# Performance work log

Measured on AMD Instinct MI355X. Metric: run time of the kernel, lower is better.

## Reference

```python
import jax, jax.numpy as jnp
import numpy as np

B, S, H = 1, 2048, 2048
NH = 16            # num attention heads
QLR = 1536         # q_lora_rank
KVLR = 512         # kv_lora_rank
DR = 64            # qk_rope_head_dim
DN = 128           # qk_nope_head_dim
DV = 128           # v_head_dim
DQK = DN + DR      # qk_head_dim = 192
EPS = 1e-6


def rmsnorm(x, w):
    xf = x.astype(jnp.float32)
    var = jnp.mean(xf * xf, axis=-1, keepdims=True)
    return (xf * jax.lax.rsqrt(var + EPS)).astype(x.dtype) * w


def rotate_half(x):
    d = x.shape[-1] // 2
    return jnp.concatenate([-x[..., d:], x[..., :d]], axis=-1)


def rope_interleave(x, cos, sin):
    # x: [b, h, s, d]; de-interleave pairs (even dims -> first half, odd -> second)
    b, h, s, d = x.shape
    x = x.reshape(b, h, s, d // 2, 2).swapaxes(-1, -2).reshape(b, h, s, d)
    return x * cos + rotate_half(x) * sin


def setup_inputs() -> dict:
    key = jax.random.key(0)
    ks = jax.random.split(key, 8)
    std = 0.02
    hidden_states = jax.random.normal(ks[0], (B, S, H), jnp.float32)
    # real rotary cos/sin for a 64-dim rope slice
    pos = jnp.arange(S, dtype=jnp.float32)
    inv_freq = 1.0 / (10000.0 ** (jnp.arange(0, DR, 2, dtype=jnp.float32) / DR))
    ang = pos[:, None] * inv_freq[None, :]            # [S, DR//2]
    emb = jnp.concatenate([ang, ang], axis=-1)        # [S, DR]
    cos = jnp.broadcast_to(jnp.cos(emb)[None], (B, S, DR)).astype(jnp.float32)
    sin = jnp.broadcast_to(jnp.sin(emb)[None], (B, S, DR)).astype(jnp.float32)
    # weights stored [in, out]
    wq_a = jax.random.normal(ks[1], (H, QLR), jnp.float32) * std
    q_ln = jnp.ones((QLR,), jnp.float32)
    wq_b = jax.random.normal(ks[2], (QLR, NH * DQK), jnp.float32) * std
    wkv_a = jax.random.normal(ks[3], (H, KVLR + DR), jnp.float32) * std
    kv_ln = jnp.ones((KVLR,), jnp.float32)
    wkv_b = jax.random.normal(ks[4], (KVLR, NH * (DN + DV)), jnp.float32) * std
    wo = jax.random.normal(ks[5], (NH * DV, H), jnp.float32) * std
    return {"hidden_states": hidden_states, "cos": cos, "sin": sin,
            "wq_a": wq_a, "q_ln": q_ln, "wq_b": wq_b,
            "wkv_a": wkv_a, "kv_ln": kv_ln, "wkv_b": wkv_b, "wo": wo}


def reference(hidden_states, cos, sin, wq_a, q_ln, wq_b, wkv_a, kv_ln, wkv_b, wo):
    b, s, _ = hidden_states.shape
    # low-rank Q: a-proj -> RMSNorm -> b-proj
    q = rmsnorm(hidden_states @ wq_a, q_ln) @ wq_b           # [b, s, NH*DQK]
    q = q.reshape(b, s, NH, DQK).transpose(0, 2, 1, 3)       # [b, NH, s, DQK]
    q_pass, q_rot = q[..., :DN], q[..., DN:]
    # compressed KV with shared rope key
    ckv = hidden_states @ wkv_a                               # [b, s, KVLR+DR]
    kv_c, k_rot = ckv[..., :KVLR], ckv[..., KVLR:]
    kv = (rmsnorm(kv_c, kv_ln) @ wkv_b).reshape(b, s, NH, DN + DV).transpose(0, 2, 1, 3)
    k_pass, v = kv[..., :DN], kv[..., DN:]
    k_rot = k_rot[:, None, :, :]                              # [b, 1, s, DR]
    cos4, sin4 = cos[:, None], sin[:, None]
    q_rot = rope_interleave(q_rot, cos4, sin4)
    k_rot = rope_interleave(k_rot, cos4, sin4)
    k_rot = jnp.broadcast_to(k_rot, (b, NH, s, DR))
    qs = jnp.concatenate([q_pass, q_rot], axis=-1)            # [b, NH, s, DQK]
    ks_ = jnp.concatenate([k_pass, k_rot], axis=-1)
    scaling = DQK ** -0.5
    scores = jnp.einsum('bhqd,bhkd->bhqk', qs, ks_) * scaling
    causal = jnp.tril(jnp.ones((s, s), bool))
    scores = jnp.where(causal, scores, jnp.finfo(scores.dtype).min)
    probs = jax.nn.softmax(scores.astype(jnp.float32), axis=-1).astype(qs.dtype)
    out = jnp.einsum('bhqk,bhkd->bhqd', probs, v)             # [b, NH, s, DV]
    out = out.transpose(0, 2, 1, 3).reshape(b, s, NH * DV)
    return out @ wo
```

## Files before the change

### kernel.cpp

```cpp
#include <hip/hip_runtime.h>
#include <hip/hip_bf16.h>
#include <stdint.h>

#define S_    2048
#define H_    2048
#define NH_   16
#define QLR_  1536
#define KVLR_ 512
#define DR_   64
#define DN_   128
#define DV_   128
#define DQK_  192
#define QW_   (NH_*DQK_)
#define KVW_  (NH_*(DN_+DV_))
#define CKVW_ (KVLR_+DR_)

typedef __attribute__((ext_vector_type(8))) short short8;
typedef __attribute__((ext_vector_type(4))) float floatx4;

__device__ __forceinline__ unsigned short f2bf(float f) {
    unsigned u = __float_as_uint(f);
    unsigned r = u + 0x7fffu + ((u >> 16) & 1u);
    return (unsigned short)(r >> 16);
}
__device__ __forceinline__ float bf2f(unsigned short h) {
    return __uint_as_float(((unsigned)h) << 16);
}
__device__ __forceinline__ void store_out(float* p, float v) { *p = v; }
__device__ __forceinline__ void store_out(unsigned short* p, float v) { *p = f2bf(v); }

typedef const __attribute__((address_space(1))) unsigned int* gas_ptr;
typedef __attribute__((address_space(3))) unsigned int* las_ptr;
__device__ __forceinline__ void gload16(const void* g, void* l) {
    __builtin_amdgcn_global_load_lds((gas_ptr)g, (las_ptr)l, 16, 0, 0);
}

__device__ __forceinline__ int xcd_swz(int orig, int nwg) {
    int q8 = nwg >> 3, r8 = nwg & 7;
    int xcd = orig & 7, jj = orig >> 3;
    return (xcd < r8 ? xcd * (q8 + 1) : r8 * (q8 + 1) + (xcd - r8) * q8) + jj;
}

#define GEMM_STAGE(b, k0) do {                                               \
        _Pragma("unroll")                                                    \
        for (int sub = 0; sub < 2; ++sub) {                                  \
            int m = tid >> 2, k8 = tid & 3;                                  \
            gload16(A + (size_t)(bm + m) * lda + (k0) + sub * 32 + k8 * 8,   \
                    &As[b][sub][tid * 8]);                                   \
        }                                                                    \
        _Pragma("unroll")                                                    \
        for (int sub = 0; sub < 2; ++sub)                                    \
            _Pragma("unroll")                                                \
            for (int j = 0; j < BN / 64; ++j) {                              \
                int ch = j * 256 + tid;                                      \
                int n = ch >> 2, k8 = ch & 3;                                \
                int nrow = bn + n; if (nrow >= N) nrow = N - 1;              \
                gload16(Bt + (size_t)nrow * K + (k0) + sub * 32 + k8 * 8,    \
                        &Bs[b][sub][ch * 8]);                                \
            }                                                                \
    } while (0)

#define GEMM_COMPUTE_SUB(sub) do {                                           \
        short8 a[2], b[NFR];                                                 \
        _Pragma("unroll")                                                    \
        for (int mi = 0; mi < 2; ++mi)                                       \
            a[mi] = *(const short8*)&As[cur][sub][(wm + mi * 16 + cc) * 32 + g * 8]; \
        _Pragma("unroll")                                                    \
        for (int ni = 0; ni < NFR; ++ni)                                     \
            b[ni] = *(const short8*)&Bs[cur][sub][(wn + ni * 16 + cc) * 32 + g * 8]; \
        __builtin_amdgcn_s_setprio(1);                                       \
        _Pragma("unroll")                                                    \
        for (int mi = 0; mi < 2; ++mi)                                       \
            _Pragma("unroll")                                                \
            for (int ni = 0; ni < NFR; ++ni)                                 \
                acc[mi][ni] = __builtin_amdgcn_mfma_f32_16x16x32_bf16(       \
                    a[mi], b[ni], acc[mi][ni], 0, 0, 0);                     \
        __builtin_amdgcn_s_setprio(0);                                       \
    } while (0)

template <typename OutT, int BN>
__global__ __launch_bounds__(256) void gemm_bf16_db(
    const unsigned short* __restrict__ A, const unsigned short* __restrict__ Bt,
    OutT* __restrict__ C, int M, int N, int K, int lda, int ldc)
{
    constexpr int NFR = BN / 32;
    __shared__ unsigned short As[2][2][64 * 32];
    __shared__ unsigned short Bs[2][2][BN * 32];

    const int tid = threadIdx.x;
    const int l = tid & 63;
    const int g = l >> 4, cc = l & 15;
    const int w = tid >> 6;
    const int wm = (w >> 1) * 32, wn = (w & 1) * (BN / 2);

    const int nwg = gridDim.x * gridDim.y;
    const int wg = xcd_swz(blockIdx.y * gridDim.x + blockIdx.x, nwg);
    const int bm = (wg / gridDim.x) * 64;
    const int bn = (wg % gridDim.x) * BN;

    floatx4 acc[2][NFR];
#pragma unroll
    for (int i = 0; i < 2; i++)
#pragma unroll
        for (int j = 0; j < NFR; j++) acc[i][j] = (floatx4){0.f, 0.f, 0.f, 0.f};

    GEMM_STAGE(0, 0);
    __syncthreads();
    int cur = 0;

    for (int k0 = 0; k0 < K; k0 += 64) {
        if (k0 + 64 < K) GEMM_STAGE(cur ^ 1, k0 + 64);
        GEMM_COMPUTE_SUB(0);
        GEMM_COMPUTE_SUB(1);
        __syncthreads();
        cur ^= 1;
    }

#pragma unroll
    for (int mi = 0; mi < 2; ++mi)
#pragma unroll
        for (int ni = 0; ni < NFR; ++ni)
#pragma unroll
            for (int i = 0; i < 4; ++i) {
                int row = bm + wm + mi * 16 + g * 4 + i;
                int col = bn + wn + ni * 16 + cc;
                if (col < N) store_out(&C[(size_t)row * ldc + col], acc[mi][ni][i]);
            }
}

__global__ __launch_bounds__(256) void gemm_bf16_dual(
    const unsigned short* __restrict__ A, const unsigned short* __restrict__ Bt,
    float* __restrict__ C0, float* __restrict__ C1,
    int M, int N, int K, int lda, int ldc0, int ldc1)
{
    constexpr int BN = 128;
    constexpr int NFR = 4;
    __shared__ unsigned short As[2][2][64 * 32];
    __shared__ unsigned short Bs[2][2][BN * 32];

    const int tid = threadIdx.x;
    const int l = tid & 63;
    const int g = l >> 4, cc = l & 15;
    const int w = tid >> 6;
    const int wm = (w >> 1) * 32, wn = (w & 1) * (BN / 2);

    const int nwg = gridDim.x * gridDim.y;
    const int wg = xcd_swz(blockIdx.y * gridDim.x + blockIdx.x, nwg);
    const int bm = (wg / gridDim.x) * 64;
    const int bn = (wg % gridDim.x) * BN;

    floatx4 acc[2][NFR];
#pragma unroll
    for (int i = 0; i < 2; i++)
#pragma unroll
        for (int j = 0; j < NFR; j++) acc[i][j] = (floatx4){0.f, 0.f, 0.f, 0.f};

    GEMM_STAGE(0, 0);
    __syncthreads();
    int cur = 0;

    for (int k0 = 0; k0 < K; k0 += 64) {
        if (k0 + 64 < K) GEMM_STAGE(cur ^ 1, k0 + 64);
        GEMM_COMPUTE_SUB(0);
        GEMM_COMPUTE_SUB(1);
        __syncthreads();
        cur ^= 1;
    }

#pragma unroll
    for (int mi = 0; mi < 2; ++mi)
#pragma unroll
        for (int ni = 0; ni < NFR; ++ni)
#pragma unroll
            for (int i = 0; i < 4; ++i) {
                int row = bm + wm + mi * 16 + g * 4 + i;
                int col = bn + wn + ni * 16 + cc;
                if (col < QLR_)
                    C0[(size_t)row * ldc0 + col] = acc[mi][ni][i];
                else if (col < N)
                    C1[(size_t)row * ldc1 + (col - QLR_)] = acc[mi][ni][i];
            }
}

__global__ __launch_bounds__(256) void gemm_bf16_pair(
    const unsigned short* __restrict__ A0, const unsigned short* __restrict__ Bt0,
    unsigned short* __restrict__ Cp0, int N0, int K0, int lda0, int ldc0, int gx0, int nwg0,
    const unsigned short* __restrict__ A1, const unsigned short* __restrict__ Bt1,
    unsigned short* __restrict__ Cp1, int N1, int K1, int lda1, int ldc1, int gx1, int nwg1)
{
    constexpr int BN = 128;
    constexpr int NFR = 4;
    __shared__ unsigned short As[2][2][64 * 32];
    __shared__ unsigned short Bs[2][2][BN * 32];

    const int tid = threadIdx.x;
    const int l = tid & 63;
    const int g = l >> 4, cc = l & 15;
    const int w = tid >> 6;
    const int wm = (w >> 1) * 32, wn = (w & 1) * (BN / 2);

    const int bid = blockIdx.x;
    const unsigned short *A, *Bt;
    unsigned short* C;
    int N, K, lda, ldc, wg, gx;
    if (bid < nwg0) {
        wg = xcd_swz(bid, nwg0); gx = gx0;
        A = A0; Bt = Bt0; C = Cp0; N = N0; K = K0; lda = lda0; ldc = ldc0;
    } else {
        wg = xcd_swz(bid - nwg0, nwg1); gx = gx1;
        A = A1; Bt = Bt1; C = Cp1; N = N1; K = K1; lda = lda1; ldc = ldc1;
    }
    const int bm = (wg / gx) * 64;
    const int bn = (wg % gx) * BN;

    floatx4 acc[2][NFR];
#pragma unroll
    for (int i = 0; i < 2; i++)
#pragma unroll
        for (int j = 0; j < NFR; j++) acc[i][j] = (floatx4){0.f, 0.f, 0.f, 0.f};

    GEMM_STAGE(0, 0);
    __syncthreads();
    int cur = 0;

    for (int k0 = 0; k0 < K; k0 += 64) {
        if (k0 + 64 < K) GEMM_STAGE(cur ^ 1, k0 + 64);
        GEMM_COMPUTE_SUB(0);
        GEMM_COMPUTE_SUB(1);
        __syncthreads();
        cur ^= 1;
    }

#pragma unroll
    for (int mi = 0; mi < 2; ++mi)
#pragma unroll
        for (int ni = 0; ni < NFR; ++ni)
#pragma unroll
            for (int i = 0; i < 4; ++i) {
                int row = bm + wm + mi * 16 + g * 4 + i;
                int col = bn + wn + ni * 16 + cc;
                if (col < N) C[(size_t)row * ldc + col] = f2bf(acc[mi][ni][i]);
            }
}

__global__ __launch_bounds__(256) void cast_bf16(
    const float* __restrict__ in, unsigned short* __restrict__ out, int n)
{
    int i = (blockIdx.x * 256 + threadIdx.x) * 4;
    if (i >= n) return;
    float4 v = *(const float4*)&in[i];
    ushort4 u;
    u.x = f2bf(v.x); u.y = f2bf(v.y); u.z = f2bf(v.z); u.w = f2bf(v.w);
    *(ushort4*)&out[i] = u;
}

__global__ __launch_bounds__(256) void transpose_cast(
    const float* __restrict__ W, unsigned short* __restrict__ Wt, int K, int N,
    float scl)
{
    __shared__ float t[32][33];
    const int n0 = blockIdx.x * 32, k0 = blockIdx.y * 32;
    const int tx = threadIdx.x & 31, ty4 = (threadIdx.x >> 5) * 4;
#pragma unroll
    for (int j = 0; j < 4; ++j)
        t[ty4 + j][tx] = W[(size_t)(k0 + ty4 + j) * N + n0 + tx];
    __syncthreads();
#pragma unroll
    for (int j = 0; j < 4; ++j)
        Wt[(size_t)(n0 + ty4 + j) * K + k0 + tx] = f2bf(t[tx][ty4 + j] * scl);
}

__global__ __launch_bounds__(256) void rmsnorm_bf16out(
    const float* __restrict__ x, const float* __restrict__ w,
    unsigned short* __restrict__ y, int cols, int xstride)
{
    const float* xr = x + (size_t)blockIdx.x * xstride;
    unsigned short* yr = y + (size_t)blockIdx.x * cols;
    const int tid = threadIdx.x;
    float ss = 0.f;
    for (int c = tid; c < cols; c += 256) { float v = xr[c]; ss += v * v; }
#pragma unroll
    for (int off = 32; off > 0; off >>= 1) ss += __shfl_xor(ss, off);
    __shared__ float red[4];
    if ((tid & 63) == 0) red[tid >> 6] = ss;
    __syncthreads();
    ss = red[0] + red[1] + red[2] + red[3];
    const float inv = rsqrtf(ss / (float)cols + 1e-6f);
    for (int c = tid; c < cols; c += 256) yr[c] = f2bf(xr[c] * inv * w[c]);
}

__global__ void rope_q_bf(unsigned short* __restrict__ q,
                          const float* __restrict__ cs, const float* __restrict__ sn)
{
    int t = blockIdx.x * 256 + threadIdx.x;
    int chunk = t >> 5, j = t & 31;
    int s = chunk >> 4, h = chunk & 15;
    unsigned short* x = q + (size_t)s * QW_ + h * DQK_ + DN_;
    float e = bf2f(x[2 * j]), o = bf2f(x[2 * j + 1]);
    float c = cs[s * DR_ + j], si = sn[s * DR_ + j];
    unsigned short u = f2bf(e * c - o * si);
    unsigned short v = f2bf(o * c + e * si);
    x[j] = u; x[j + 32] = v;
}

__global__ __launch_bounds__(256) void prep_k(
    const unsigned short* __restrict__ kvb, const float* __restrict__ ckv,
    const float* __restrict__ cs, const float* __restrict__ sn,
    unsigned short* __restrict__ kg)
{
    const int s = blockIdx.x, tid = threadIdx.x;
    __shared__ unsigned short rot[64];
    if (tid < 32) {
        int j = tid;
        const float* x = ckv + (size_t)s * CKVW_ + KVLR_;
        float e = x[2 * j], o = x[2 * j + 1];
        float c = cs[s * DR_ + j], si = sn[s * DR_ + j];
        rot[j] = f2bf(e * c - o * si);
        rot[j + 32] = f2bf(o * c + e * si);
    }
    __syncthreads();
    const int sw = s & 7;
    for (int ch = tid; ch < 384; ch += 256) {
        int hh = ch / 24, d8 = ch % 24;
        short8 v;
        if (d8 < 16)
            v = *(const short8*)&kvb[(size_t)s * KVW_ + hh * 256 + d8 * 8];
        else
            v = *(const short8*)&rot[(d8 - 16) * 8];
        int d8s = d8 ^ sw;
        *(short8*)&kg[((size_t)hh * S_ + s) * 192 + d8s * 8] = v;
    }
}

__global__ __launch_bounds__(256) void transpose_v(
    const unsigned short* __restrict__ kvb, unsigned short* __restrict__ vt)
{
    __shared__ unsigned short t[32][36];
    const int dv0 = blockIdx.x * 32, s0 = blockIdx.y * 32, h = blockIdx.z;
    const int r = threadIdx.x >> 3, c4 = threadIdx.x & 7;
    ushort4 ld = *(const ushort4*)&kvb[(size_t)(s0 + r) * KVW_ + h * 256 + 128 + dv0 + c4 * 4];
    t[r][c4 * 4 + 0] = ld.x; t[r][c4 * 4 + 1] = ld.y;
    t[r][c4 * 4 + 2] = ld.z; t[r][c4 * 4 + 3] = ld.w;
    __syncthreads();
    ushort4 st;
    st.x = t[c4 * 4 + 0][r]; st.y = t[c4 * 4 + 1][r];
    st.z = t[c4 * 4 + 2][r]; st.w = t[c4 * 4 + 3][r];
    *(ushort4*)&vt[(size_t)(h * 128 + dv0 + r) * S_ + s0 + c4 * 4] = st;
}

__global__ __launch_bounds__(512, 4) void flash_attn9(
    const unsigned short* __restrict__ qg, const unsigned short* __restrict__ kg,
    const unsigned short* __restrict__ vt,
    unsigned short* __restrict__ op0, unsigned short* __restrict__ op1,
    float* __restrict__ mlp)
{
    const int bid = blockIdx.x;
    const int j = 15 - (bid >> 5);
    const int low5 = bid & 31;
    const int h = low5 & 15;
    const int sp = low5 >> 4;
    const int pb = h * 16 + j;

    __shared__ unsigned short sm[2 * 6144 + 2 * 4096 + 8 * 640];
    unsigned short* Kb = sm;
    unsigned short* Vb = sm + 12288;
    const int tid = threadIdx.x;
    const int w = tid >> 6;
    const int l = tid & 63, g = l >> 4, cc = l & 15;
    unsigned short* Pw = sm + 20480 + w * 640;

    const int qmin = j * 128 + w * 16;
    const int q_lane = qmin + cc;
    const int wave_qmax = qmin + 15;
    const int cnt = 2 * (j + 1);
    const int kt_begin = sp * cnt, kt_end = kt_begin + cnt;

    const unsigned short* kh = kg + (size_t)h * S_ * 192;
    const unsigned short* vh = vt + (size_t)(h * 128) * S_;

    short8 qf[6];
    {
        const unsigned short* qb = qg + (size_t)q_lane * QW_ + h * DQK_;
#pragma unroll
        for (int k6 = 0; k6 < 6; ++k6)
            qf[k6] = *(const short8*)&qb[k6 * 32 + g * 8];
    }

    floatx4 accO[8];
#pragma unroll
    for (int nt = 0; nt < 8; ++nt) accO[nt] = (floatx4){0.f, 0.f, 0.f, 0.f};
    float m_r = -1e30f, l_r = 0.f;

#define STAGE_KV(b, kt) do {                                             \
        const unsigned short* ksrc = kh + (size_t)(kt) * 32 * 192;       \
        gload16(ksrc + tid * 8, Kb + (b) * 6144 + tid * 8);              \
        if (tid < 256)                                                   \
            gload16(ksrc + (512 + tid) * 8,                              \
                    Kb + (b) * 6144 + (512 + tid) * 8);                  \
        const int krow = (kt) * 32;                                      \
        {                                                                \
            int dv = tid >> 2, j8 = tid & 3;                             \
            gload16(vh + (size_t)dv * S_ + krow + j8 * 8,                \
                    Vb + (b) * 4096 + tid * 8);                          \
        }                                                                \
    } while (0)

    STAGE_KV(0, kt_begin);
    int cur = 0;

    for (int kt = kt_begin; kt < kt_end; ++kt) {
        const int krow0 = kt * 32;
        __syncthreads();
        if (kt + 1 < kt_end) STAGE_KV(cur ^ 1, kt + 1);

        if (krow0 <= wave_qmax) {
            const unsigned short* Kc = Kb + cur * 6144;
            const unsigned short* Vc = Vb + cur * 4096;
            const int swz = (cc & 7) << 3;

            floatx4 s0 = (floatx4){0.f, 0.f, 0.f, 0.f};
            floatx4 s1 = (floatx4){0.f, 0.f, 0.f, 0.f};
            __builtin_amdgcn_s_setprio(1);
#pragma unroll
            for (int k6 = 0; k6 < 6; ++k6) {
                short8 b0 = *(const short8*)&Kc[cc * 192 + ((k6 * 32 + g * 8) ^ swz)];
                short8 b1 = *(const short8*)&Kc[(16 + cc) * 192 + ((k6 * 32 + g * 8) ^ swz)];
                s0 = __builtin_amdgcn_mfma_f32_16x16x32_bf16(b0, qf[k6], s0, 0, 0, 0);
                s1 = __builtin_amdgcn_mfma_f32_16x16x32_bf16(b1, qf[k6], s1, 0, 0, 0);
            }
            __builtin_amdgcn_s_setprio(0);

            float v0[4], v1[4];
            if (krow0 + 31 <= qmin) {
#pragma unroll
                for (int i = 0; i < 4; ++i) { v0[i] = s0[i]; v1[i] = s1[i]; }
            } else {
#pragma unroll
                for (int i = 0; i < 4; ++i) {
                    v0[i] = (krow0 + g * 4 + i) <= q_lane ? s0[i] : -1e30f;
                    v1[i] = (krow0 + 16 + g * 4 + i) <= q_lane ? s1[i] : -1e30f;
                }
            }
            float mt = fmaxf(fmaxf(fmaxf(v0[0], v0[1]), fmaxf(v0[2], v0[3])),
                             fmaxf(fmaxf(v1[0], v1[1]), fmaxf(v1[2], v1[3])));
            mt = fmaxf(mt, __shfl_xor(mt, 16));
            mt = fmaxf(mt, __shfl_xor(mt, 32));

            if (!__all(mt <= m_r + 6.0f)) {
                float mn = fmaxf(m_r, mt);
                float alpha = exp2f(m_r - mn);
                m_r = mn;
                l_r *= alpha;
                float aB[4];
#pragma unroll
                for (int i = 0; i < 4; ++i) aB[i] = __shfl(alpha, g * 4 + i);
#pragma unroll
                for (int nt = 0; nt < 8; ++nt)
#pragma unroll
                    for (int i = 0; i < 4; ++i) accO[nt][i] *= aB[i];
            }

            float p0[4], p1[4], ps = 0.f;
#pragma unroll
            for (int i = 0; i < 4; ++i) {
                p0[i] = exp2f(v0[i] - m_r);
                p1[i] = exp2f(v1[i] - m_r);
                ps += p0[i] + p1[i];
            }
            ps += __shfl_xor(ps, 16);
            ps += __shfl_xor(ps, 32);
            l_r += ps;

            {
                unsigned pk00, pk01, pk10, pk11;
                asm("v_cvt_pk_bf16_f32 %0, %1, %2" : "=v"(pk00) : "v"(p0[0]), "v"(p0[1]));
                asm("v_cvt_pk_bf16_f32 %0, %1, %2" : "=v"(pk01) : "v"(p0[2]), "v"(p0[3]));
                asm("v_cvt_pk_bf16_f32 %0, %1, %2" : "=v"(pk10) : "v"(p1[0]), "v"(p1[1]));
                asm("v_cvt_pk_bf16_f32 %0, %1, %2" : "=v"(pk11) : "v"(p1[2]), "v"(p1[3]));
                uint2 w0, w1;
                w0.x = pk00; w0.y = pk01;
                w1.x = pk10; w1.y = pk11;
                *(uint2*)&Pw[cc * 40 + g * 4] = w0;
                *(uint2*)&Pw[cc * 40 + 16 + g * 4] = w1;
            }

            short8 pf = *(const short8*)&Pw[cc * 40 + g * 8];
            __builtin_amdgcn_s_setprio(1);
#pragma unroll
            for (int nt = 0; nt < 8; ++nt) {
                short8 vr = *(const short8*)&Vc[(nt * 16 + cc) * 32 + g * 8];
                accO[nt] = __builtin_amdgcn_mfma_f32_16x16x32_bf16(pf, vr, accO[nt], 0, 0, 0);
            }
            __builtin_amdgcn_s_setprio(0);
        }
        cur ^= 1;
    }
#undef STAGE_KV

    float mB[4], lB[4];
#pragma unroll
    for (int i = 0; i < 4; ++i) {
        int src = (g << 4) | (g * 4 + i);
        mB[i] = __shfl(m_r, src);
        lB[i] = __shfl(l_r, src);
    }
    unsigned short* op = sp ? op1 : op0;
#pragma unroll
    for (int nt = 0; nt < 8; ++nt)
#pragma unroll
        for (int i = 0; i < 4; ++i)
            op[(size_t)pb * 16384 + (w * 16 + g * 4 + i) * 128 + nt * 16 + cc] =
                f2bf(accO[nt][i]);
    if (cc == 0) {
#pragma unroll
        for (int i = 0; i < 4; ++i) {
            size_t mi = ((size_t)(sp * 256 + pb) * 128 + w * 16 + g * 4 + i) * 2;
            mlp[mi + 0] = mB[i];
            mlp[mi + 1] = lB[i];
        }
    }
}

__global__ __launch_bounds__(256) void merge_attn9(
    const unsigned short* __restrict__ op0, const unsigned short* __restrict__ op1,
    const float* __restrict__ mlp, unsigned short* __restrict__ ao)
{
    const int bid = blockIdx.x;
    const int pb = bid >> 1;
    const int rh = (bid & 1) * 64;
    const int h = pb >> 4, j = pb & 15;
    const int tid = threadIdx.x;
    const int row = rh + (tid >> 2), c0 = (tid & 3) * 32;

    const size_t mi0 = ((size_t)pb * 128 + row) * 2;
    const size_t mi1 = ((size_t)(256 + pb) * 128 + row) * 2;
    float m0 = mlp[mi0 + 0], l0 = mlp[mi0 + 1];
    float m1 = mlp[mi1 + 0], l1 = mlp[mi1 + 1];
    float mf = fmaxf(m0, m1);
    float e0 = exp2f(m0 - mf), e1 = exp2f(m1 - mf);
    float inv = 1.f / (l0 * e0 + l1 * e1);
    float w0 = e0 * inv, w1 = e1 * inv;

    const size_t pbase = (size_t)pb * 16384 + row * 128 + c0;
    unsigned short* dst = ao + (size_t)(j * 128 + row) * (NH_ * DV_) + h * DV_ + c0;
#pragma unroll
    for (int s = 0; s < 4; ++s) {
        short8 a = *(const short8*)&op0[pbase + s * 8];
        short8 b = *(const short8*)&op1[pbase + s * 8];
        short8 o;
#pragma unroll
        for (int k = 0; k < 8; ++k)
            o[k] = (short)f2bf(bf2f((unsigned short)a[k]) * w0 +
                               bf2f((unsigned short)b[k]) * w1);
        *(short8*)&dst[s * 8] = o;
    }
}

extern "C" void kernel_launch(void* const* d_in, const int* in_sizes, int n_in,
                              void* d_out, int out_size, void* d_ws, size_t ws_size,
                              hipStream_t stream)
{
    const float* hs    = (const float*)d_in[0];
    const float* cosp  = (const float*)d_in[1];
    const float* sinp  = (const float*)d_in[2];
    const float* wq_a  = (const float*)d_in[3];
    const float* q_ln  = (const float*)d_in[4];
    const float* wq_b  = (const float*)d_in[5];
    const float* wkv_a = (const float*)d_in[6];
    const float* kv_ln = (const float*)d_in[7];
    const float* wkv_b = (const float*)d_in[8];
    const float* wo    = (const float*)d_in[9];
    float* out = (float*)d_out;

    char* ws = (char*)d_ws;
    float*          qa     = (float*)(ws);
    float*          ckv    = (float*)(ws + 12582912);
    unsigned short* q_bf   = (unsigned short*)(ws + 17301504);
    unsigned short* kvb    = (unsigned short*)(ws + 29884416);
    unsigned short* hs_bf  = (unsigned short*)(ws + 46661632);
    unsigned short* qa_bf  = (unsigned short*)(ws + 55050240);
    unsigned short* ckv_bf = (unsigned short*)(ws + 61341696);
    unsigned short* ao_bf  = (unsigned short*)(ws + 63438848);
    unsigned short* wt     = (unsigned short*)(ws + 71827456);
    unsigned short* kg     = (unsigned short*)qa;
    unsigned short* vtb    = hs_bf;
    unsigned short* wbt2   = (unsigned short*)qa;

    unsigned short* op0 = qa_bf;
    unsigned short* op1 = wt;
    float*          mlp = ckv;

    const float qscale = 0.07216878364870322f * 1.4426950408889634f;

    cast_bf16<<<(S_ * H_) / 1024, 256, 0, stream>>>(hs, hs_bf, S_ * H_);

    transpose_cast<<<dim3(QLR_ / 32, H_ / 32), 256, 0, stream>>>(wq_a, wt, H_, QLR_, 1.f);
    transpose_cast<<<dim3(CKVW_ / 32, H_ / 32), 256, 0, stream>>>(
        wkv_a, wt + (size_t)QLR_ * H_, H_, CKVW_, 1.f);
    gemm_bf16_dual<<<dim3((QLR_ + CKVW_ + 127) / 128, S_ / 64), 256, 0, stream>>>(
        hs_bf, wt, qa, ckv, S_, QLR_ + CKVW_, H_, H_, QLR_, CKVW_);
    rmsnorm_bf16out<<<S_, 256, 0, stream>>>(qa, q_ln, qa_bf, QLR_, QLR_);
    rmsnorm_bf16out<<<S_, 256, 0, stream>>>(ckv, kv_ln, ckv_bf, KVLR_, CKVW_);

    transpose_cast<<<dim3(QW_ / 32, QLR_ / 32), 256, 0, stream>>>(wq_b, wt, QLR_, QW_, qscale);
    transpose_cast<<<dim3(KVW_ / 32, KVLR_ / 32), 256, 0, stream>>>(wkv_b, wbt2, KVLR_, KVW_, 1.f);
    gemm_bf16_pair<<<768 + 1024, 256, 0, stream>>>(
        qa_bf, wt, q_bf, QW_, QLR_, QLR_, QW_, QW_ / 128, 768,
        ckv_bf, wbt2, kvb, KVW_, KVLR_, KVLR_, KVW_, KVW_ / 128, 1024);
    rope_q_bf<<<(S_ * NH_ * 32) / 256, 256, 0, stream>>>(q_bf, cosp, sinp);

    prep_k<<<S_, 256, 0, stream>>>(kvb, ckv, cosp, sinp, kg);
    transpose_v<<<dim3(4, 64, 16), 256, 0, stream>>>(kvb, vtb);

    flash_attn9<<<512, 512, 0, stream>>>(q_bf, kg, vtb, op0, op1, mlp);
    merge_attn9<<<512, 256, 0, stream>>>(op0, op1, mlp, ao_bf);

    transpose_cast<<<dim3(H_ / 32, H_ / 32), 256, 0, stream>>>(wo, wt, H_, H_, 1.f);
    gemm_bf16_db<float, 128><<<dim3(H_ / 128, S_ / 64), 256, 0, stream>>>(
        ao_bf, wt, out, S_, H_, NH_ * DV_, NH_ * DV_, H_);
}
```

Baseline: 218.2 us.

## Shrink attention query blocks to 64 rows and pass P via shuffles

Changes the flash attention kernel from 128-query blocks with 8 waves to 64-query blocks with 4 waves, doubling the grid to 1024 blocks and updating the split-K partial-output and merge indexing to match. The probability tile is now redistributed across lanes with cross-lane shuffles rather than written to and re-read from LDS, which removes the per-wave P staging buffer. The aim is finer-grained work for causal load balance, higher occupancy, and less LDS traffic. In exchange each block stages the same K/V tiles for fewer queries, so K/V reuse drops and global load traffic rises.

```diff
diff --git a/kernel.cpp b/kernel.cpp
--- a/kernel.cpp
+++ b/kernel.cpp
@@ -348,32 +348,31 @@
     *(ushort4*)&vt[(size_t)(h * 128 + dv0 + r) * S_ + s0 + c4 * 4] = st;
 }
 
-__global__ __launch_bounds__(512, 4) void flash_attn9(
+__global__ __launch_bounds__(256, 4) void flash_attn7(
     const unsigned short* __restrict__ qg, const unsigned short* __restrict__ kg,
     const unsigned short* __restrict__ vt,
     unsigned short* __restrict__ op0, unsigned short* __restrict__ op1,
     float* __restrict__ mlp)
 {
     const int bid = blockIdx.x;
-    const int j = 15 - (bid >> 5);
+    const int qblk = 31 - (bid >> 5);
     const int low5 = bid & 31;
     const int h = low5 & 15;
     const int sp = low5 >> 4;
-    const int pb = h * 16 + j;
-
-    __shared__ unsigned short sm[2 * 6144 + 2 * 4096 + 8 * 640];
+    const int pb = h * 32 + qblk;
+
+    __shared__ unsigned short sm[2 * 6144 + 2 * 4096];
     unsigned short* Kb = sm;
     unsigned short* Vb = sm + 12288;
     const int tid = threadIdx.x;
     const int w = tid >> 6;
     const int l = tid & 63, g = l >> 4, cc = l & 15;
-    unsigned short* Pw = sm + 20480 + w * 640;
-
-    const int qmin = j * 128 + w * 16;
+
+    const int qmin = qblk * 64 + w * 16;
     const int q_lane = qmin + cc;
     const int wave_qmax = qmin + 15;
-    const int cnt = 2 * (j + 1);
-    const int kt_begin = sp * cnt, kt_end = kt_begin + cnt;
+    const int HT = qblk + 1;
+    const int kt_begin = sp * HT, kt_end = kt_begin + HT;
 
     const unsigned short* kh = kg + (size_t)h * S_ * 192;
     const unsigned short* vh = vt + (size_t)(h * 128) * S_;
@@ -393,15 +392,18 @@
 
 #define STAGE_KV(b, kt) do {                                             \
         const unsigned short* ksrc = kh + (size_t)(kt) * 32 * 192;       \
-        gload16(ksrc + tid * 8, Kb + (b) * 6144 + tid * 8);              \
-        if (tid < 256)                                                   \
-            gload16(ksrc + (512 + tid) * 8,                              \
-                    Kb + (b) * 6144 + (512 + tid) * 8);                  \
+        _Pragma("unroll")                                                \
+        for (int j = 0; j < 3; ++j) {                                    \
+            int ch = j * 256 + tid;                                      \
+            gload16(ksrc + ch * 8, Kb + (b) * 6144 + ch * 8);            \
+        }                                                                \
         const int krow = (kt) * 32;                                      \
-        {                                                                \
-            int dv = tid >> 2, j8 = tid & 3;                             \
+        _Pragma("unroll")                                                \
+        for (int j = 0; j < 2; ++j) {                                    \
+            int ch = j * 256 + tid;                                      \
+            int dv = ch >> 2, j8 = ch & 3;                               \
             gload16(vh + (size_t)dv * S_ + krow + j8 * 8,                \
-                    Vb + (b) * 4096 + tid * 8);                          \
+                    Vb + (b) * 4096 + ch * 8);                           \
         }                                                                \
     } while (0)
 
@@ -471,20 +473,28 @@
             ps += __shfl_xor(ps, 32);
             l_r += ps;
 
+            short8 pf;
             {
                 unsigned pk00, pk01, pk10, pk11;
                 asm("v_cvt_pk_bf16_f32 %0, %1, %2" : "=v"(pk00) : "v"(p0[0]), "v"(p0[1]));
                 asm("v_cvt_pk_bf16_f32 %0, %1, %2" : "=v"(pk01) : "v"(p0[2]), "v"(p0[3]));
                 asm("v_cvt_pk_bf16_f32 %0, %1, %2" : "=v"(pk10) : "v"(p1[0]), "v"(p1[1]));
                 asm("v_cvt_pk_bf16_f32 %0, %1, %2" : "=v"(pk11) : "v"(p1[2]), "v"(p1[3]));
-                uint2 w0, w1;
-                w0.x = pk00; w0.y = pk01;
-                w1.x = pk10; w1.y = pk11;
-                *(uint2*)&Pw[cc * 40 + g * 4] = w0;
-                *(uint2*)&Pw[cc * 40 + 16 + g * 4] = w1;
-            }
-
-            short8 pf = *(const short8*)&Pw[cc * 40 + g * 8];
+                const int lA = ((g & 1) << 5) | cc;
+                const int lB = lA | 16;
+                unsigned a0 = __shfl((int)pk00, lA), a1 = __shfl((int)pk01, lA);
+                unsigned b0 = __shfl((int)pk00, lB), b1 = __shfl((int)pk01, lB);
+                unsigned c0 = __shfl((int)pk10, lA), c1 = __shfl((int)pk11, lA);
+                unsigned d0 = __shfl((int)pk10, lB), d1 = __shfl((int)pk11, lB);
+                const bool lo = g < 2;
+                uint4 pw;
+                pw.x = lo ? a0 : c0;
+                pw.y = lo ? a1 : c1;
+                pw.z = lo ? b0 : d0;
+                pw.w = lo ? b1 : d1;
+                pf = *(short8*)&pw;
+            }
+
             __builtin_amdgcn_s_setprio(1);
 #pragma unroll
             for (int nt = 0; nt < 8; ++nt) {
@@ -497,43 +507,41 @@
     }
 #undef STAGE_KV
 
-    float mB[4], lB[4];
+    float mB[4], lB4[4];
 #pragma unroll
     for (int i = 0; i < 4; ++i) {
         int src = (g << 4) | (g * 4 + i);
         mB[i] = __shfl(m_r, src);
-        lB[i] = __shfl(l_r, src);
+        lB4[i] = __shfl(l_r, src);
     }
     unsigned short* op = sp ? op1 : op0;
 #pragma unroll
     for (int nt = 0; nt < 8; ++nt)
 #pragma unroll
         for (int i = 0; i < 4; ++i)
-            op[(size_t)pb * 16384 + (w * 16 + g * 4 + i) * 128 + nt * 16 + cc] =
+            op[(size_t)pb * 8192 + (w * 16 + g * 4 + i) * 128 + nt * 16 + cc] =
                 f2bf(accO[nt][i]);
     if (cc == 0) {
 #pragma unroll
         for (int i = 0; i < 4; ++i) {
-            size_t mi = ((size_t)(sp * 256 + pb) * 128 + w * 16 + g * 4 + i) * 2;
+            size_t mi = ((size_t)(sp * 512 + pb) * 64 + w * 16 + g * 4 + i) * 2;
             mlp[mi + 0] = mB[i];
-            mlp[mi + 1] = lB[i];
+            mlp[mi + 1] = lB4[i];
         }
     }
 }
 
-__global__ __launch_bounds__(256) void merge_attn9(
+__global__ __launch_bounds__(256) void merge_attn(
     const unsigned short* __restrict__ op0, const unsigned short* __restrict__ op1,
     const float* __restrict__ mlp, unsigned short* __restrict__ ao)
 {
-    const int bid = blockIdx.x;
-    const int pb = bid >> 1;
-    const int rh = (bid & 1) * 64;
-    const int h = pb >> 4, j = pb & 15;
+    const int pb = blockIdx.x;
+    const int h = pb >> 5, qblk = pb & 31;
     const int tid = threadIdx.x;
-    const int row = rh + (tid >> 2), c0 = (tid & 3) * 32;
-
-    const size_t mi0 = ((size_t)pb * 128 + row) * 2;
-    const size_t mi1 = ((size_t)(256 + pb) * 128 + row) * 2;
+    const int row = tid >> 2, c0 = (tid & 3) * 32;
+
+    const size_t mi0 = ((size_t)pb * 64 + row) * 2;
+    const size_t mi1 = ((size_t)(512 + pb) * 64 + row) * 2;
     float m0 = mlp[mi0 + 0], l0 = mlp[mi0 + 1];
     float m1 = mlp[mi1 + 0], l1 = mlp[mi1 + 1];
     float mf = fmaxf(m0, m1);
@@ -541,18 +549,18 @@
     float inv = 1.f / (l0 * e0 + l1 * e1);
     float w0 = e0 * inv, w1 = e1 * inv;
 
-    const size_t pbase = (size_t)pb * 16384 + row * 128 + c0;
-    unsigned short* dst = ao + (size_t)(j * 128 + row) * (NH_ * DV_) + h * DV_ + c0;
-#pragma unroll
-    for (int s = 0; s < 4; ++s) {
-        short8 a = *(const short8*)&op0[pbase + s * 8];
-        short8 b = *(const short8*)&op1[pbase + s * 8];
+    const size_t pbase = (size_t)pb * 8192 + row * 128 + c0;
+    unsigned short* dst = ao + (size_t)(qblk * 64 + row) * (NH_ * DV_) + h * DV_ + c0;
+#pragma unroll
+    for (int j = 0; j < 4; ++j) {
+        short8 a = *(const short8*)&op0[pbase + j * 8];
+        short8 b = *(const short8*)&op1[pbase + j * 8];
         short8 o;
 #pragma unroll
         for (int k = 0; k < 8; ++k)
             o[k] = (short)f2bf(bf2f((unsigned short)a[k]) * w0 +
                                bf2f((unsigned short)b[k]) * w1);
-        *(short8*)&dst[s * 8] = o;
+        *(short8*)&dst[j * 8] = o;
     }
 }
 
@@ -612,8 +620,8 @@
     prep_k<<<S_, 256, 0, stream>>>(kvb, ckv, cosp, sinp, kg);
     transpose_v<<<dim3(4, 64, 16), 256, 0, stream>>>(kvb, vtb);
 
-    flash_attn9<<<512, 512, 0, stream>>>(q_bf, kg, vtb, op0, op1, mlp);
-    merge_attn9<<<512, 256, 0, stream>>>(op0, op1, mlp, ao_bf);
+    flash_attn7<<<1024, 256, 0, stream>>>(q_bf, kg, vtb, op0, op1, mlp);
+    merge_attn<<<512, 256, 0, stream>>>(op0, op1, mlp, ao_bf);
 
     transpose_cast<<<dim3(H_ / 32, H_ / 32), 256, 0, stream>>>(wo, wt, H_, H_, 1.f);
     gemm_bf16_db<float, 128><<<dim3(H_ / 128, S_ / 64), 256, 0, stream>>>(
```

Result: no change. 221.5 us (+1.5%).
